# Kernel tuning notes

Measured on AMD Instinct MI355X. Metric: run time of the kernel, lower is better.

## Reference

```python
import jax, jax.numpy as jnp
import numpy as np

N = 50000      # num_nodes
E = 800000     # num_edges
D_IN = 128
D_HID = 128
D_EMB = 128
G = 4          # num_gcns
BN_EPS = 1e-5


def setup_inputs() -> dict:
    key = jax.random.key(0)
    ks = jax.random.split(key, 8)
    x = jax.random.normal(ks[0], (N, D_IN), dtype=jnp.float32)
    edge_index = jax.random.randint(ks[1], (2, E), 0, N, dtype=jnp.int64)
    # per-GCN params, stacked on leading G axis
    W1 = jax.random.normal(ks[2], (G, D_IN, D_HID), dtype=jnp.float32) / np.sqrt(D_IN)
    b1 = jnp.zeros((G, D_HID), dtype=jnp.float32)
    W2 = jax.random.normal(ks[3], (G, D_HID, D_EMB), dtype=jnp.float32) / np.sqrt(D_HID)
    b2 = jnp.zeros((G, D_EMB), dtype=jnp.float32)
    gamma1 = jnp.ones((G, D_HID), dtype=jnp.float32)
    beta1 = jnp.zeros((G, D_HID), dtype=jnp.float32)
    gamma2 = jnp.ones((G, D_EMB), dtype=jnp.float32)
    beta2 = jnp.zeros((G, D_EMB), dtype=jnp.float32)
    alpha = jnp.asarray(0.25, dtype=jnp.float32)  # PReLU (single shared param)
    mix_embed = jnp.full((N, G), 1.0 / G, dtype=jnp.float32)
    return {"x": x, "edge_index": edge_index, "W1": W1, "b1": b1, "W2": W2,
            "b2": b2, "gamma1": gamma1, "beta1": beta1, "gamma2": gamma2,
            "beta2": beta2, "alpha": alpha, "mix_embed": mix_embed}


def _gcn_norm(edge_index, num_nodes):
    # PyG GCNConv: add self-loops, symmetric normalization D^-1/2 (A+I) D^-1/2
    row, col = edge_index[0], edge_index[1]
    loop = jnp.arange(num_nodes, dtype=edge_index.dtype)
    row = jnp.concatenate([row, loop])
    col = jnp.concatenate([col, loop])
    w = jnp.ones(row.shape[0], dtype=jnp.float32)
    deg = jax.ops.segment_sum(w, col, num_segments=num_nodes)
    dinv = jnp.where(deg > 0, deg ** -0.5, 0.0)
    norm = dinv[row] * w * dinv[col]
    return row, col, norm


def _propagate(h, row, col, norm, num_nodes):
    # gather from source, scale by edge norm, scatter-add to target
    msg = h[row] * norm[:, None]
    return jax.ops.segment_sum(msg, col, num_segments=num_nodes)


def _batchnorm(z, gamma, beta):
    mu = jnp.mean(z, axis=0)
    var = jnp.mean((z - mu) ** 2, axis=0)  # biased, as torch BN training mode
    return (z - mu) * jax.lax.rsqrt(var + BN_EPS) * gamma + beta


def _prelu(z, alpha):
    return jnp.where(z > 0, z, alpha * z)


def reference(x, edge_index, W1, b1, W2, b2, gamma1, beta1, gamma2, beta2, alpha, mix_embed):
    num_nodes = x.shape[0]
    row, col, norm = _gcn_norm(edge_index, num_nodes)
    mix = jax.nn.softmax(mix_embed, axis=-1)  # [N, G]
    out = jnp.zeros((num_nodes, D_EMB), dtype=x.dtype)
    for g in range(G):  # small fixed number of mixture components
        h = x @ W1[g]
        z = _propagate(h, row, col, norm, num_nodes) + b1[g]
        z = _prelu(_batchnorm(z, gamma1[g], beta1[g]), alpha)
        h = z @ W2[g]
        z = _propagate(h, row, col, norm, num_nodes) + b2[g]
        z = _prelu(_batchnorm(z, gamma2[g], beta2[g]), alpha)
        out = out + mix[:, g:g + 1] * z
    return out
```

## Files before the change

### kernel.cpp

```cpp
#include <hip/hip_runtime.h>
#include <stdint.h>

static constexpr float EPS = 1e-5f;

typedef __attribute__((ext_vector_type(8))) short bfrag;
typedef __attribute__((ext_vector_type(4))) float ffrag;

__device__ __forceinline__ float bf2f(unsigned short u){
  union { unsigned int i; float f; } v; v.i = ((unsigned int)u) << 16; return v.f;
}
__device__ __forceinline__ unsigned short f2bf(float f){
  union { float f; unsigned int i; } v; v.f = f;
  unsigned int x = v.i;
  x += 0x7fffu + ((x >> 16) & 1u);
  return (unsigned short)(x >> 16);
}
__device__ __forceinline__ float lo16(unsigned int v){ return bf2f((unsigned short)(v & 0xffffu)); }
__device__ __forceinline__ float hi16(unsigned int v){ return bf2f((unsigned short)(v >> 16)); }
__device__ __forceinline__ unsigned int pack2(float a, float b){
  return ((unsigned int)f2bf(b) << 16) | (unsigned int)f2bf(a);
}

__global__ void k_deg(const int* __restrict__ col, int* __restrict__ indeg, int N, int E){
  int e = blockIdx.x * 256 + threadIdx.x;
  if (e < E){
    unsigned c = (unsigned)col[e];
    if (c < (unsigned)N) atomicAdd(&indeg[c], 1);
  }
}

__global__ void k_alloc(const int* __restrict__ indeg, int* __restrict__ ctr,
                        int* __restrict__ offs, int* __restrict__ cursor,
                        float* __restrict__ dinv, int N){
  int tid = blockIdx.x * 256 + threadIdx.x;
  int lane = threadIdx.x & 63;
  int v = (tid < N) ? indeg[tid] : 0;
  int incl = v;
  #pragma unroll
  for (int d = 1; d < 64; d <<= 1){
    int u = __shfl_up(incl, d);
    if (lane >= d) incl += u;
  }
  int base = 0;
  if (lane == 63) base = atomicAdd(ctr, incl);
  base = __shfl(base, 63);
  if (tid < N){
    int o = base + incl - v;
    offs[tid] = o; cursor[tid] = o;
    dinv[tid] = rsqrtf((float)(v + 1));
  }
}

__global__ void k_scatter(const int* __restrict__ row, const int* __restrict__ col,
                          int* __restrict__ cursor, int* __restrict__ csr, int N, int E){
  int e = blockIdx.x * 256 + threadIdx.x;
  if (e < E){
    unsigned c = (unsigned)col[e];
    if (c < (unsigned)N){
      int p = atomicAdd(&cursor[c], 1);
      unsigned r = (unsigned)row[e];
      csr[p] = (r < (unsigned)N) ? (int)r : 0;
    }
  }
}

__global__ void k_prep(const float* __restrict__ x, const float* __restrict__ dinv,
                       unsigned short* __restrict__ xs,
                       const float* __restrict__ W1, const float* __restrict__ W2,
                       unsigned short* __restrict__ Wt1, unsigned short* __restrict__ Wt2,
                       int total4x){
  int b = blockIdx.x;
  if (b < 512){
    int idx = b * 256 + threadIdx.x;
    const float* W = W1; unsigned short* Wt = Wt1;
    if (idx >= 65536){ idx -= 65536; W = W2; Wt = Wt2; }
    int c = idx >> 7, k = idx & 127;
    int g = c >> 7, j = c & 127;
    Wt[(size_t)c * 128 + k] = f2bf(W[(size_t)g*16384 + k*128 + j]);
  } else {
    int idx = (b - 512) * 256 + threadIdx.x;
    int stride = (gridDim.x - 512) * 256;
    for (; idx < total4x; idx += stride){
      int i = idx >> 5;
      float di = dinv[i];
      float4 v = ((const float4*)x)[idx];
      ushort4 o;
      o.x = f2bf(di * v.x); o.y = f2bf(di * v.y);
      o.z = f2bf(di * v.z); o.w = f2bf(di * v.w);
      ((ushort4*)xs)[idx] = o;
    }
  }
}

__global__ __launch_bounds__(256) void k_prop_x(const unsigned int* __restrict__ xs2,
                                               const int* __restrict__ csr,
                                               const int* __restrict__ offs, const int* __restrict__ indeg,
                                               const float* __restrict__ dinv,
                                               unsigned int* __restrict__ s2, int N){
  int i = blockIdx.x * 4 + (threadIdx.x >> 6);
  if (i >= N) return;
  int c2 = threadIdx.x & 63;
  unsigned int sv = xs2[(size_t)i*64 + c2];
  float ax = lo16(sv), ay = hi16(sv);
  int e = offs[i], end = e + indeg[i];
  for (; e + 8 <= end; e += 8){
    int r0 = csr[e], r1 = csr[e+1], r2 = csr[e+2], r3 = csr[e+3];
    int r4 = csr[e+4], r5 = csr[e+5], r6 = csr[e+6], r7 = csr[e+7];
    unsigned int v0 = xs2[(size_t)r0*64 + c2], v1 = xs2[(size_t)r1*64 + c2];
    unsigned int v2 = xs2[(size_t)r2*64 + c2], v3 = xs2[(size_t)r3*64 + c2];
    unsigned int v4 = xs2[(size_t)r4*64 + c2], v5 = xs2[(size_t)r5*64 + c2];
    unsigned int v6 = xs2[(size_t)r6*64 + c2], v7 = xs2[(size_t)r7*64 + c2];
    ax += lo16(v0)+lo16(v1)+lo16(v2)+lo16(v3)+lo16(v4)+lo16(v5)+lo16(v6)+lo16(v7);
    ay += hi16(v0)+hi16(v1)+hi16(v2)+hi16(v3)+hi16(v4)+hi16(v5)+hi16(v6)+hi16(v7);
  }
  for (; e < end; e++){
    unsigned int v = xs2[(size_t)csr[e]*64 + c2];
    ax += lo16(v); ay += hi16(v);
  }
  float di = dinv[i];
  s2[(size_t)i*64 + c2] = pack2(di * ax, di * ay);
}

__global__ __launch_bounds__(256) void k_gram(const unsigned short* __restrict__ in,
                                              int rstride, int coff128,
                                              float* __restrict__ Gbase, float* __restrict__ msumbase,
                                              int N){
  int gy = blockIdx.y;
  const unsigned short* src = in + gy * coff128;
  float* G = Gbase + (size_t)gy * 16384;
  float* msum = msumbase + gy * 128;

  __shared__ unsigned short st[128 * 40];
  __shared__ float colsum[128];

  int t = threadIdx.x;
  int wv = t >> 6, lane = t & 63, l16 = lane & 15, quad = lane >> 4;
  if (t < 128) colsum[t] = 0.f;

  int sn = t & 31, scb = t >> 5;

  ffrag acc[2][8];
  #pragma unroll
  for (int a = 0; a < 2; a++)
    #pragma unroll
    for (int b = 0; b < 8; b++) acc[a][b] = (ffrag){0.f,0.f,0.f,0.f};

  float cs[16];
  #pragma unroll
  for (int j = 0; j < 16; j++) cs[j] = 0.f;

  for (int c0 = blockIdx.x * 32; c0 < N; c0 += gridDim.x * 32){
    __syncthreads();
    int n = c0 + sn;
    ushort4 u0, u1, u2, u3;
    if (n < N){
      const ushort4* p = (const ushort4*)(src + (size_t)n * rstride + scb * 16);
      u0 = p[0]; u1 = p[1]; u2 = p[2]; u3 = p[3];
    } else {
      u0 = u1 = u2 = u3 = (ushort4){0,0,0,0};
    }
    unsigned short vals[16] = {u0.x,u0.y,u0.z,u0.w, u1.x,u1.y,u1.z,u1.w,
                               u2.x,u2.y,u2.z,u2.w, u3.x,u3.y,u3.z,u3.w};
    #pragma unroll
    for (int j = 0; j < 16; j++){
      st[(scb * 16 + j) * 40 + sn] = vals[j];
      cs[j] += bf2f(vals[j]);
    }
    __syncthreads();
    #pragma unroll
    for (int ta = 0; ta < 2; ta++){
      int ra = wv * 2 + ta;
      bfrag af = *(const bfrag*)&st[(ra * 16 + l16) * 40 + quad * 8];
      #pragma unroll
      for (int tb = 0; tb < 8; tb++){
        bfrag bf = *(const bfrag*)&st[(tb * 16 + l16) * 40 + quad * 8];
        acc[ta][tb] = __builtin_amdgcn_mfma_f32_16x16x32_bf16(af, bf, acc[ta][tb], 0, 0, 0);
      }
    }
  }
  #pragma unroll
  for (int j = 0; j < 16; j++) atomicAdd(&colsum[scb * 16 + j], cs[j]);
  __syncthreads();
  if (t < 128) atomicAdd(&msum[t], colsum[t]);
  #pragma unroll
  for (int ta = 0; ta < 2; ta++){
    #pragma unroll
    for (int tb = 0; tb < 8; tb++){
      int row0 = wv * 32 + ta * 16 + quad * 4;
      int colg = tb * 16 + l16;
      #pragma unroll
      for (int r = 0; r < 4; r++)
        atomicAdd(&G[(size_t)(row0 + r) * 128 + colg], acc[ta][tb][r]);
    }
  }
}

__global__ __launch_bounds__(64) void k_bnfit(const float* __restrict__ W,
                                              const float* __restrict__ gamma, const float* __restrict__ beta,
                                              const float* __restrict__ Gbase, int gmul,
                                              const float* __restrict__ msumbase, int mmul,
                                              float* __restrict__ scale, float* __restrict__ shiftF,
                                              float invN){
  int c = blockIdx.x;
  int g = c >> 7, j = c & 127;
  const float* Wc = W + (size_t)g * 16384 + j;
  const float* G  = Gbase + (size_t)g * gmul;
  const float* mv = msumbase + g * mmul;
  __shared__ float wl[128];
  __shared__ float ml[128];
  int t = threadIdx.x;
  for (int k = t; k < 128; k += 64){ wl[k] = Wc[(size_t)k * 128]; ml[k] = mv[k] * invN; }
  __syncthreads();
  float quad = 0.f, dm = 0.f;
  #pragma unroll
  for (int kk = 0; kk < 2; kk++){
    int k = t + kk * 64;
    float wk = wl[k];
    dm += ml[k] * wk;
    const float* Gr = G + (size_t)k * 128;
    float p = 0.f;
    for (int jj = 0; jj < 128; jj += 4){
      float4 gg = *(const float4*)(Gr + jj);
      float4 ww = *(const float4*)(wl + jj);
      p += gg.x*ww.x + gg.y*ww.y + gg.z*ww.z + gg.w*ww.w;
    }
    quad += wk * p;
  }
  for (int o = 32; o > 0; o >>= 1){
    quad += __shfl_down(quad, o);
    dm   += __shfl_down(dm, o);
  }
  if (t == 0){
    float var = quad * invN - dm * dm;
    float sc = gamma[c] * rsqrtf(var + EPS);
    scale[c] = sc;
    shiftF[c] = beta[c] - dm * sc;
  }
}

__global__ __launch_bounds__(256) void k_mm1f(const unsigned short* __restrict__ in,
                                              const unsigned short* __restrict__ Wt,
                                              const float* __restrict__ scale, const float* __restrict__ shiftF,
                                              const float* __restrict__ alpha_p, const float* __restrict__ dinv,
                                              unsigned short* __restrict__ h, int N){
  float alpha = alpha_p[0];
  int wave = threadIdx.x >> 6, lane = threadIdx.x & 63;
  int l16 = lane & 15, quad = lane >> 4;
  int node = blockIdx.x * 16 + l16;
  int nc = node < N ? node : N - 1;
  int colbase0 = wave * 128;
  float di = dinv[nc];

  const unsigned short* inrow = in + (size_t)nc * 128 + quad * 8;
  bfrag b0 = *(const bfrag*)(inrow);
  bfrag b1 = *(const bfrag*)(inrow + 32);
  bfrag b2 = *(const bfrag*)(inrow + 64);
  bfrag b3 = *(const bfrag*)(inrow + 96);

  #pragma unroll
  for (int ct = 0; ct < 8; ct++){
    int colbase = colbase0 + ct * 16;
    const unsigned short* wrow = Wt + (size_t)(colbase + l16) * 128 + quad * 8;
    bfrag a0 = *(const bfrag*)(wrow);
    bfrag a1 = *(const bfrag*)(wrow + 32);
    bfrag a2 = *(const bfrag*)(wrow + 64);
    bfrag a3 = *(const bfrag*)(wrow + 96);
    ffrag acc = {0.f, 0.f, 0.f, 0.f};
    acc = __builtin_amdgcn_mfma_f32_16x16x32_bf16(a0, b0, acc, 0, 0, 0);
    acc = __builtin_amdgcn_mfma_f32_16x16x32_bf16(a1, b1, acc, 0, 0, 0);
    acc = __builtin_amdgcn_mfma_f32_16x16x32_bf16(a2, b2, acc, 0, 0, 0);
    acc = __builtin_amdgcn_mfma_f32_16x16x32_bf16(a3, b3, acc, 0, 0, 0);
    int cb = colbase + quad * 4;
    float4 sc = *(const float4*)(scale + cb);
    float4 sh = *(const float4*)(shiftF + cb);
    float v0 = acc[0]*sc.x + sh.x; v0 = v0 > 0.f ? v0 : alpha*v0;
    float v1 = acc[1]*sc.y + sh.y; v1 = v1 > 0.f ? v1 : alpha*v1;
    float v2 = acc[2]*sc.z + sh.z; v2 = v2 > 0.f ? v2 : alpha*v2;
    float v3 = acc[3]*sc.w + sh.w; v3 = v3 > 0.f ? v3 : alpha*v3;
    uint2 o;
    o.x = pack2(di*v0, di*v1);
    o.y = pack2(di*v2, di*v3);
    if (node < N)
      *(uint2*)(h + (size_t)node * 512 + cb) = o;
  }
}

__global__ __launch_bounds__(256) void k_prop_h(const unsigned int* __restrict__ h2,
                                                const int* __restrict__ csr,
                                                const int* __restrict__ offs, const int* __restrict__ indeg,
                                                const float* __restrict__ dinv,
                                                unsigned int* __restrict__ t2, int N){
  int B = blockIdx.x;
  int s = B & 7, g = B >> 3;
  int i = g * 8 + (threadIdx.x >> 5);
  if (i >= N) return;
  int c2 = s * 32 + (threadIdx.x & 31);
  unsigned int sv = h2[(size_t)i*256 + c2];
  float ax = lo16(sv), ay = hi16(sv);
  int e = offs[i], end = e + indeg[i];
  for (; e + 8 <= end; e += 8){
    int r0 = csr[e], r1 = csr[e+1], r2 = csr[e+2], r3 = csr[e+3];
    int r4 = csr[e+4], r5 = csr[e+5], r6 = csr[e+6], r7 = csr[e+7];
    unsigned int v0 = h2[(size_t)r0*256 + c2], v1 = h2[(size_t)r1*256 + c2];
    unsigned int v2 = h2[(size_t)r2*256 + c2], v3 = h2[(size_t)r3*256 + c2];
    unsigned int v4 = h2[(size_t)r4*256 + c2], v5 = h2[(size_t)r5*256 + c2];
    unsigned int v6 = h2[(size_t)r6*256 + c2], v7 = h2[(size_t)r7*256 + c2];
    ax += lo16(v0)+lo16(v1)+lo16(v2)+lo16(v3)+lo16(v4)+lo16(v5)+lo16(v6)+lo16(v7);
    ay += hi16(v0)+hi16(v1)+hi16(v2)+hi16(v3)+hi16(v4)+hi16(v5)+hi16(v6)+hi16(v7);
  }
  for (; e < end; e++){
    unsigned int v = h2[(size_t)csr[e]*256 + c2];
    ax += lo16(v); ay += hi16(v);
  }
  float di = dinv[i];
  t2[(size_t)i*256 + c2] = pack2(di * ax, di * ay);
}

__global__ __launch_bounds__(256) void k_mm2f(const unsigned short* __restrict__ t,
                                              const unsigned short* __restrict__ Wt,
                                              const float* __restrict__ scale, const float* __restrict__ shiftF,
                                              const float* __restrict__ alpha_p, const float* __restrict__ mixe,
                                              float* __restrict__ out, int N){
  __shared__ float red[4][16][132];
  float alpha = alpha_p[0];
  int wave = threadIdx.x >> 6, lane = threadIdx.x & 63;
  int l16 = lane & 15, quad = lane >> 4;
  int node = blockIdx.x * 16 + l16;
  int nc = node < N ? node : N - 1;

  float4 me = ((const float4*)mixe)[nc];
  float mx = fmaxf(fmaxf(me.x, me.y), fmaxf(me.z, me.w));
  float e0 = __expf(me.x - mx), e1 = __expf(me.y - mx), e2 = __expf(me.z - mx), e3 = __expf(me.w - mx);
  float inv = 1.f / (e0 + e1 + e2 + e3);
  float wvx = ((wave == 0) ? e0 : (wave == 1) ? e1 : (wave == 2) ? e2 : e3) * inv;

  const unsigned short* inrow = t + (size_t)nc * 512 + wave * 128 + quad * 8;
  bfrag b0 = *(const bfrag*)(inrow);
  bfrag b1 = *(const bfrag*)(inrow + 32);
  bfrag b2 = *(const bfrag*)(inrow + 64);
  bfrag b3 = *(const bfrag*)(inrow + 96);

  #pragma unroll
  for (int ct = 0; ct < 8; ct++){
    int c512 = wave * 128 + ct * 16;
    const unsigned short* wrow = Wt + (size_t)(c512 + l16) * 128 + quad * 8;
    bfrag a0 = *(const bfrag*)(wrow);
    bfrag a1 = *(const bfrag*)(wrow + 32);
    bfrag a2 = *(const bfrag*)(wrow + 64);
    bfrag a3 = *(const bfrag*)(wrow + 96);
    ffrag acc = {0.f, 0.f, 0.f, 0.f};
    acc = __builtin_amdgcn_mfma_f32_16x16x32_bf16(a0, b0, acc, 0, 0, 0);
    acc = __builtin_amdgcn_mfma_f32_16x16x32_bf16(a1, b1, acc, 0, 0, 0);
    acc = __builtin_amdgcn_mfma_f32_16x16x32_bf16(a2, b2, acc, 0, 0, 0);
    acc = __builtin_amdgcn_mfma_f32_16x16x32_bf16(a3, b3, acc, 0, 0, 0);
    int cb = c512 + quad * 4;
    float4 sc = *(const float4*)(scale + cb);
    float4 sh = *(const float4*)(shiftF + cb);
    float v0 = acc[0]*sc.x + sh.x; v0 = v0 > 0.f ? v0 : alpha*v0;
    float v1 = acc[1]*sc.y + sh.y; v1 = v1 > 0.f ? v1 : alpha*v1;
    float v2 = acc[2]*sc.z + sh.z; v2 = v2 > 0.f ? v2 : alpha*v2;
    float v3 = acc[3]*sc.w + sh.w; v3 = v3 > 0.f ? v3 : alpha*v3;
    int j = ct * 16 + quad * 4;
    float4 wr = {wvx*v0, wvx*v1, wvx*v2, wvx*v3};
    *(float4*)&red[wave][l16][j] = wr;
  }
  __syncthreads();
  int tt = threadIdx.x;
  int nn = tt >> 4, j0 = (tt & 15) * 8;
  int gnode = blockIdx.x * 16 + nn;
  if (gnode < N){
    float4 r0 = {0,0,0,0}, r1 = {0,0,0,0};
    #pragma unroll
    for (int w = 0; w < 4; w++){
      float4 p0 = *(const float4*)&red[w][nn][j0];
      float4 p1 = *(const float4*)&red[w][nn][j0 + 4];
      r0.x += p0.x; r0.y += p0.y; r0.z += p0.z; r0.w += p0.w;
      r1.x += p1.x; r1.y += p1.y; r1.z += p1.z; r1.w += p1.w;
    }
    float* op = out + (size_t)gnode * 128 + j0;
    *(float4*)(op) = r0;
    *(float4*)(op + 4) = r1;
  }
}

extern "C" void kernel_launch(void* const* d_in, const int* in_sizes, int n_in,
                              void* d_out, int out_size, void* d_ws, size_t ws_size,
                              hipStream_t stream) {
  const float* x      = (const float*)d_in[0];
  const int*   ei     = (const int*)d_in[1];
  const float* W1     = (const float*)d_in[2];
  const float* W2     = (const float*)d_in[4];
  const float* gamma1 = (const float*)d_in[6];
  const float* beta1  = (const float*)d_in[7];
  const float* gamma2 = (const float*)d_in[8];
  const float* beta2  = (const float*)d_in[9];
  const float* alpha  = (const float*)d_in[10];
  const float* mixe   = (const float*)d_in[11];
  float* out = (float*)d_out;

  const int N = in_sizes[0] / 128;
  const int E = in_sizes[1] / 2;
  const int* rowv = ei;
  const int* colv = ei + E;

  char* w = (char*)d_ws;
  size_t off = 0;
  auto take = [&](size_t bytes) -> void* {
    void* p = w + off;
    off = (off + bytes + 255) & ~(size_t)255;
    return p;
  };
  size_t zbeg = off;
  int*   indeg  = (int*)take((size_t)N * 4);
  int*   ctr    = (int*)take(256);
  float* G1     = (float*)take(65536);
  float* G2     = (float*)take(262144);
  float* m1     = (float*)take(512);
  float* m2     = (float*)take(2048);
  size_t zend = off;
  int*   cursor = (int*)take((size_t)N * 4);
  int*   offs   = (int*)take((size_t)N * 4);
  float* dinv   = (float*)take((size_t)N * 4);
  float* scale1 = (float*)take(2048);
  float* shift1 = (float*)take(2048);
  float* scale2 = (float*)take(2048);
  float* shift2 = (float*)take(2048);
  int*   csr    = (int*)take((size_t)E * 4);
  unsigned short* Wt1 = (unsigned short*)take(512 * 128 * 2);
  unsigned short* Wt2 = (unsigned short*)take(512 * 128 * 2);
  unsigned short* xs = (unsigned short*)take((size_t)N * 128 * 2);
  unsigned short* sb = (unsigned short*)take((size_t)N * 128 * 2);
  unsigned short* h  = (unsigned short*)take((size_t)N * 512 * 2);
  unsigned short* tb = (unsigned short*)take((size_t)N * 512 * 2);

  hipMemsetAsync((char*)d_ws + zbeg, 0, zend - zbeg, stream);

  int ebl = (E + 255) / 256;
  int nb  = (N + 255) / 256;
  float invN = 1.0f / (float)N;

  k_deg<<<ebl, 256, 0, stream>>>(colv, indeg, N, E);
  k_alloc<<<nb, 256, 0, stream>>>(indeg, ctr, offs, cursor, dinv, N);
  k_scatter<<<ebl, 256, 0, stream>>>(rowv, colv, cursor, csr, N, E);

  k_prep<<<512 + 1024, 256, 0, stream>>>(x, dinv, xs, W1, W2, Wt1, Wt2, N * 32);
  k_prop_x<<<(N + 3) / 4, 256, 0, stream>>>((const unsigned int*)xs, csr, offs, indeg, dinv, (unsigned int*)sb, N);

  k_gram<<<dim3(32, 1), 256, 0, stream>>>(sb, 128, 0, G1, m1, N);
  k_bnfit<<<512, 64, 0, stream>>>(W1, gamma1, beta1, G1, 0, m1, 0, scale1, shift1, invN);
  k_mm1f<<<(N + 15) / 16, 256, 0, stream>>>(sb, Wt1, scale1, shift1, alpha, dinv, h, N);

  k_prop_h<<<((N + 7) / 8) * 8, 256, 0, stream>>>((const unsigned int*)h, csr, offs, indeg, dinv, (unsigned int*)tb, N);

  k_gram<<<dim3(32, 4), 256, 0, stream>>>(tb, 512, 128, G2, m2, N);
  k_bnfit<<<512, 64, 0, stream>>>(W2, gamma2, beta2, G2, 16384, m2, 128, scale2, shift2, invN);
  k_mm2f<<<(N + 15) / 16, 256, 0, stream>>>(tb, Wt2, scale2, shift2, alpha, mixe, out, N);
}
```

Before: 624.2 us.

## Fold prep work into degree/scatter kernels and restructure second propagation per node

Weight transposition moves into the degree-count kernel and the x pre-scaling moves into the CSR scatter kernel as extra blocks, removing one launch. The degree and scatter kernels now each handle two edges per thread. The second propagation kernel now uses one 256-thread block per node covering all 512 columns, with a 16-way unrolled gather to keep more loads in flight. Per-node blocks give each block less work and add scheduling overhead, and the wider unroll raises register pressure.

```diff
diff --git a/kernel.cpp b/kernel.cpp
--- a/kernel.cpp
+++ b/kernel.cpp
@@ -21,11 +21,31 @@
   return ((unsigned int)f2bf(b) << 16) | (unsigned int)f2bf(a);
 }
 
-__global__ void k_deg(const int* __restrict__ col, int* __restrict__ indeg, int N, int E){
-  int e = blockIdx.x * 256 + threadIdx.x;
-  if (e < E){
-    unsigned c = (unsigned)col[e];
-    if (c < (unsigned)N) atomicAdd(&indeg[c], 1);
+__global__ __launch_bounds__(256) void k_deg(const int* __restrict__ col, int* __restrict__ indeg,
+                                             int N, int E, int dbl,
+                                             const float* __restrict__ W1, const float* __restrict__ W2,
+                                             unsigned short* __restrict__ Wt1, unsigned short* __restrict__ Wt2){
+  int b = blockIdx.x;
+  if (b < dbl){
+    int e0 = (b * 256 + threadIdx.x) * 2;
+    if (e0 < E){
+      if (e0 + 1 < E){
+        int2 cc = *(const int2*)&col[e0];
+        unsigned c0 = (unsigned)cc.x, c1 = (unsigned)cc.y;
+        if (c0 < (unsigned)N) atomicAdd(&indeg[c0], 1);
+        if (c1 < (unsigned)N) atomicAdd(&indeg[c1], 1);
+      } else {
+        unsigned c0 = (unsigned)col[e0];
+        if (c0 < (unsigned)N) atomicAdd(&indeg[c0], 1);
+      }
+    }
+  } else {
+    int idx = (b - dbl) * 256 + threadIdx.x;
+    const float* W = W1; unsigned short* Wt = Wt1;
+    if (idx >= 65536){ idx -= 65536; W = W2; Wt = Wt2; }
+    int c = idx >> 7, k = idx & 127;
+    int g = c >> 7, j = c & 127;
+    Wt[(size_t)c * 128 + k] = f2bf(W[(size_t)g*16384 + k*128 + j]);
   }
 }
 
@@ -51,35 +71,29 @@
   }
 }
 
-__global__ void k_scatter(const int* __restrict__ row, const int* __restrict__ col,
-                          int* __restrict__ cursor, int* __restrict__ csr, int N, int E){
-  int e = blockIdx.x * 256 + threadIdx.x;
-  if (e < E){
-    unsigned c = (unsigned)col[e];
-    if (c < (unsigned)N){
-      int p = atomicAdd(&cursor[c], 1);
-      unsigned r = (unsigned)row[e];
-      csr[p] = (r < (unsigned)N) ? (int)r : 0;
-    }
-  }
-}
-
-__global__ void k_prep(const float* __restrict__ x, const float* __restrict__ dinv,
-                       unsigned short* __restrict__ xs,
-                       const float* __restrict__ W1, const float* __restrict__ W2,
-                       unsigned short* __restrict__ Wt1, unsigned short* __restrict__ Wt2,
-                       int total4x){
+__global__ __launch_bounds__(256) void k_scatter(const int* __restrict__ row, const int* __restrict__ col,
+                                                 int* __restrict__ cursor, int* __restrict__ csr,
+                                                 int N, int E, int sbl,
+                                                 const float* __restrict__ x, const float* __restrict__ dinv,
+                                                 unsigned short* __restrict__ xs, int total4x){
   int b = blockIdx.x;
-  if (b < 512){
-    int idx = b * 256 + threadIdx.x;
-    const float* W = W1; unsigned short* Wt = Wt1;
-    if (idx >= 65536){ idx -= 65536; W = W2; Wt = Wt2; }
-    int c = idx >> 7, k = idx & 127;
-    int g = c >> 7, j = c & 127;
-    Wt[(size_t)c * 128 + k] = f2bf(W[(size_t)g*16384 + k*128 + j]);
+  if (b < sbl){
+    int e0 = (b * 256 + threadIdx.x) * 2;
+    #pragma unroll
+    for (int q = 0; q < 2; q++){
+      int e = e0 + q;
+      if (e < E){
+        unsigned c = (unsigned)col[e];
+        if (c < (unsigned)N){
+          int p = atomicAdd(&cursor[c], 1);
+          unsigned r = (unsigned)row[e];
+          csr[p] = (r < (unsigned)N) ? (int)r : 0;
+        }
+      }
+    }
   } else {
-    int idx = (b - 512) * 256 + threadIdx.x;
-    int stride = (gridDim.x - 512) * 256;
+    int idx = (b - sbl) * 256 + threadIdx.x;
+    int stride = (gridDim.x - sbl) * 256;
     for (; idx < total4x; idx += stride){
       int i = idx >> 5;
       float di = dinv[i];
@@ -290,23 +304,27 @@
                                                 const int* __restrict__ offs, const int* __restrict__ indeg,
                                                 const float* __restrict__ dinv,
                                                 unsigned int* __restrict__ t2, int N){
-  int B = blockIdx.x;
-  int s = B & 7, g = B >> 3;
-  int i = g * 8 + (threadIdx.x >> 5);
-  if (i >= N) return;
-  int c2 = s * 32 + (threadIdx.x & 31);
+  int i = blockIdx.x;
+  int c2 = threadIdx.x;
   unsigned int sv = h2[(size_t)i*256 + c2];
   float ax = lo16(sv), ay = hi16(sv);
   int e = offs[i], end = e + indeg[i];
-  for (; e + 8 <= end; e += 8){
+  for (; e + 16 <= end; e += 16){
+    int r[16];
+    #pragma unroll
+    for (int j = 0; j < 16; j++) r[j] = csr[e + j];
+    unsigned int v[16];
+    #pragma unroll
+    for (int j = 0; j < 16; j++) v[j] = h2[(size_t)r[j]*256 + c2];
+    #pragma unroll
+    for (int j = 0; j < 16; j++){ ax += lo16(v[j]); ay += hi16(v[j]); }
+  }
+  for (; e + 4 <= end; e += 4){
     int r0 = csr[e], r1 = csr[e+1], r2 = csr[e+2], r3 = csr[e+3];
-    int r4 = csr[e+4], r5 = csr[e+5], r6 = csr[e+6], r7 = csr[e+7];
     unsigned int v0 = h2[(size_t)r0*256 + c2], v1 = h2[(size_t)r1*256 + c2];
     unsigned int v2 = h2[(size_t)r2*256 + c2], v3 = h2[(size_t)r3*256 + c2];
-    unsigned int v4 = h2[(size_t)r4*256 + c2], v5 = h2[(size_t)r5*256 + c2];
-    unsigned int v6 = h2[(size_t)r6*256 + c2], v7 = h2[(size_t)r7*256 + c2];
-    ax += lo16(v0)+lo16(v1)+lo16(v2)+lo16(v3)+lo16(v4)+lo16(v5)+lo16(v6)+lo16(v7);
-    ay += hi16(v0)+hi16(v1)+hi16(v2)+hi16(v3)+hi16(v4)+hi16(v5)+hi16(v6)+hi16(v7);
+    ax += lo16(v0)+lo16(v1)+lo16(v2)+lo16(v3);
+    ay += hi16(v0)+hi16(v1)+hi16(v2)+hi16(v3);
   }
   for (; e < end; e++){
     unsigned int v = h2[(size_t)csr[e]*256 + c2];
@@ -435,22 +453,21 @@
 
   hipMemsetAsync((char*)d_ws + zbeg, 0, zend - zbeg, stream);
 
-  int ebl = (E + 255) / 256;
   int nb  = (N + 255) / 256;
+  int dbl = (E + 511) / 512;
   float invN = 1.0f / (float)N;
 
-  k_deg<<<ebl, 256, 0, stream>>>(colv, indeg, N, E);
+  k_deg<<<dbl + 512, 256, 0, stream>>>(colv, indeg, N, E, dbl, W1, W2, Wt1, Wt2);
   k_alloc<<<nb, 256, 0, stream>>>(indeg, ctr, offs, cursor, dinv, N);
-  k_scatter<<<ebl, 256, 0, stream>>>(rowv, colv, cursor, csr, N, E);
-
-  k_prep<<<512 + 1024, 256, 0, stream>>>(x, dinv, xs, W1, W2, Wt1, Wt2, N * 32);
+  k_scatter<<<dbl + 1024, 256, 0, stream>>>(rowv, colv, cursor, csr, N, E, dbl, x, dinv, xs, N * 32);
+
   k_prop_x<<<(N + 3) / 4, 256, 0, stream>>>((const unsigned int*)xs, csr, offs, indeg, dinv, (unsigned int*)sb, N);
 
   k_gram<<<dim3(32, 1), 256, 0, stream>>>(sb, 128, 0, G1, m1, N);
   k_bnfit<<<512, 64, 0, stream>>>(W1, gamma1, beta1, G1, 0, m1, 0, scale1, shift1, invN);
   k_mm1f<<<(N + 15) / 16, 256, 0, stream>>>(sb, Wt1, scale1, shift1, alpha, dinv, h, N);
 
-  k_prop_h<<<((N + 7) / 8) * 8, 256, 0, stream>>>((const unsigned int*)h, csr, offs, indeg, dinv, (unsigned int*)tb, N);
+  k_prop_h<<<N, 256, 0, stream>>>((const unsigned int*)h, csr, offs, indeg, dinv, (unsigned int*)tb, N);
 
   k_gram<<<dim3(32, 4), 256, 0, stream>>>(tb, 512, 128, G2, m2, N);
   k_bnfit<<<512, 64, 0, stream>>>(W2, gamma2, beta2, G2, 16384, m2, 128, scale2, shift2, invN);
```

After: 604.5 us. 1.03x faster.
